# Kernel optimization log

Hardware: AMD Instinct MI355X
Metric: run time of the kernel (lower is better)

The kernel has to match this reference:

```python
import jax, jax.numpy as jnp
import numpy as np

B, N, IN_DIM, H, L = 8, 1024, 3, 256, 3
NUM_STEPS = 200
LN_EPS = 1e-5


def _cdist(a, b):
    # Euclidean pairwise distance, a:[B,n,d], b:[B,m,d] -> [B,n,m]
    d2 = (jnp.sum(a * a, -1)[:, :, None] + jnp.sum(b * b, -1)[:, None, :]
          - 2.0 * jnp.einsum('bik,bjk->bij', a, b))
    d2 = jnp.maximum(d2, 0.0)
    safe = jnp.sqrt(jnp.where(d2 > 0, d2, 1.0))
    return jnp.where(d2 > 0, safe, 0.0)


def _layernorm(x, g, b):
    mu = jnp.mean(x, -1, keepdims=True)
    var = jnp.mean(jnp.square(x - mu), -1, keepdims=True)
    return (x - mu) * jax.lax.rsqrt(var + LN_EPS) * g + b


def setup_inputs() -> dict:
    key = jax.random.key(0)
    ks = jax.random.split(key, 32)
    s = 0.02
    inp = {
        'x': jax.random.normal(ks[0], (B, N, IN_DIM), jnp.float32),
        't': jax.random.randint(ks[1], (B,), 0, NUM_STEPS),
        'mask': jnp.ones((B, N), bool),
        # top-level weights (stored [in,out])
        'w_time': jax.random.normal(ks[2], (1, H)) * s,
        'b_time': jnp.zeros((H,)),
        'w_in': jax.random.normal(ks[3], (IN_DIM + H, H)) * s,
        'b_in': jnp.zeros((H,)),
        'w_out': jax.random.normal(ks[4], (H, IN_DIM)) * s,
        'b_out': jnp.zeros((IN_DIM,)),
        # per-layer stacked params [L, ...]
        'qkv_w': jax.random.normal(ks[5], (L, H, 3 * H)) * s,
        'qkv_b': jnp.zeros((L, 3 * H)),
        'ao_w': jax.random.normal(ks[6], (L, H, H)) * s,
        'ao_b': jnp.zeros((L, H)),
        'fc1_w': jax.random.normal(ks[7], (L, H, 4 * H)) * s,
        'fc1_b': jax.random.normal(ks[8], (L, 4 * H)) * s,
        'fc2_w': jax.random.normal(ks[9], (L, 4 * H, H)) * s,
        'fc2_b': jax.random.normal(ks[10], (L, H)) * s,
        'ln1_g': jnp.ones((L, H)), 'ln1_b': jnp.zeros((L, H)),
        'ln2_g': jnp.ones((L, H)), 'ln2_b': jnp.zeros((L, H)),
    }
    return inp


def reference(x, t, mask, w_time, b_time, w_in, b_in, w_out, b_out,
              qkv_w, qkv_b, ao_w, ao_b, fc1_w, fc1_b, fc2_w, fc2_b,
              ln1_g, ln1_b, ln2_g, ln2_b):
    tf = t.astype(jnp.float32)[:, None] / float(NUM_STEPS)          # [B,1]
    t_embed = jax.nn.relu(tf @ w_time + b_time)                      # [B,H]
    t_embed = jnp.broadcast_to(t_embed[:, None, :], (B, N, H))
    h = jax.nn.relu(jnp.concatenate([x, t_embed], -1) @ w_in + b_in)  # [B,N,H]
    geo = _cdist(h[:, :, :3], h[:, :, :3])                           # [B,N,N]
    mask_f = mask.astype(h.dtype)
    scale = 1.0 / jnp.sqrt(jnp.float32(H))
    for l in range(L):
        qkv = (h @ qkv_w[l] + qkv_b[l]).reshape(B, N, 3, H)
        q, k, v = qkv[:, :, 0], qkv[:, :, 1], qkv[:, :, 2]
        dist = _cdist(geo, geo)                                      # cdist of the distance matrix itself
        scores = jnp.einsum('bik,bjk->bij', q, k) * scale * jnp.exp(-dist)
        scores = jnp.where(mask[:, None, :], scores, -jnp.inf)
        attn = jax.nn.softmax(scores, axis=-1)
        ao = (jnp.einsum('bij,bjk->bik', attn, v) @ ao_w[l] + ao_b[l]) * mask_f[:, :, None]
        xx = _layernorm(h + ao, ln1_g[l], ln1_b[l])
        f1 = jax.nn.relu((xx @ fc1_w[l] + fc1_b[l]) * mask_f[:, :, None])
        ffn = jax.nn.relu((f1 @ fc2_w[l] + fc2_b[l]) * mask_f[:, :, None])
        h = _layernorm(xx + ffn, ln2_g[l], ln2_b[l])
    return (h @ w_out + b_out) * mask_f[:, :, None]
```

## Files before the change

kernel.cpp:

```cpp
#include <hip/hip_runtime.h>
#include <math.h>

#define NB 8
#define NN 1024
#define NH 256
#define NL 3

typedef unsigned short u16;
typedef __bf16 bf16x8 __attribute__((ext_vector_type(8)));
typedef _Float16 f16x8 __attribute__((ext_vector_type(8)));
typedef float f32x4 __attribute__((ext_vector_type(4)));

constexpr int EPI_BIAS_RELU = 2, EPI_BIAS_RELU_RESID = 3, EPI_EDIST = 5, EPI_QKV = 6;

__device__ __forceinline__ unsigned bf16rne(float f) {
    unsigned u = __float_as_uint(f);
    return (u + 0x7fffu + ((u >> 16) & 1u)) >> 16;
}
__device__ __forceinline__ unsigned bfpair(float a, float b) {
    return bf16rne(a) | (bf16rne(b) << 16);
}
__device__ __forceinline__ float bf2f(u16 h) {
    unsigned u = ((unsigned)h) << 16;
    return __uint_as_float(u);
}

__device__ __forceinline__ float blockSum256(float v) {
    __shared__ float sm[4];
    #pragma unroll
    for (int o = 32; o; o >>= 1) v += __shfl_down(v, o, 64);
    int lane = threadIdx.x & 63, wid = threadIdx.x >> 6;
    if (lane == 0) sm[wid] = v;
    __syncthreads();
    if (threadIdx.x == 0) sm[0] = sm[0] + sm[1] + sm[2] + sm[3];
    __syncthreads();
    float r = sm[0];
    __syncthreads();
    return r;
}

template <int EPI, int DT, bool OBF, int SWZ, int MT>
__global__ __launch_bounds__(256) void gemm_mfma(
    const u16* __restrict__ A, int lda, long sA,
    const u16* __restrict__ Bt, int ldb, long sB,
    void* __restrict__ C, int ldc, long sC,
    int K,
    const float* __restrict__ bias, long sBias,
    const float* __restrict__ resid, int ldr,
    u16* __restrict__ vtout)
{
    constexpr int MF = MT / 32;
    constexpr int ASZ = MT * 8;
    __shared__ uint4 sm4[ASZ + 1024];
    const int tid = threadIdx.x;

    int bx = blockIdx.x, by = blockIdx.y, bz = blockIdx.z;
    bool trans = false;
    if (SWZ == 2) {
        int gx = gridDim.x;
        int T = gx * gridDim.y;
        int lid = bx + gx * by;
        int nl = (lid & 7) * (T >> 3) + (lid >> 3);
        bx = nl % gx; by = nl / gx;
    } else if (SWZ == 3) {
        int lid = bx + gridDim.x * bz;
        bz = lid & 7;
        int idx = lid >> 3;
        int j = 0;
        while (idx >= 16 - 2 * j) { idx -= 16 - 2 * j; j++; }
        by = 2 * j + idx;
        bx = j;
        trans = (by >= 2 * bx + 2);
    }
    const int z = bz;
    const int row0 = by * MT, col0 = bx * 128;

    f32x4 acc[MF][4];
    #pragma unroll
    for (int m = 0; m < MF; m++)
        #pragma unroll
        for (int n = 0; n < 4; n++) acc[m][n] = (f32x4){0.f, 0.f, 0.f, 0.f};

    const int l = tid & 63, wid = tid >> 6;
    const int wr = wid >> 1, wc = wid & 1;
    const int lrow = l & 15, lgrp = l >> 4;

    for (int k0 = 0; k0 < K; k0 += 64) {
        if (MT == 128) {
            const int srow = tid >> 1, half = tid & 1, cb = half * 4, swz = srow & 7;
            const u16* Ap = A + (long)z * sA + (long)(row0 + srow) * lda + k0 + half * 32;
            uint4 a0 = *(const uint4*)(Ap + 0),  a1 = *(const uint4*)(Ap + 8);
            uint4 a2 = *(const uint4*)(Ap + 16), a3 = *(const uint4*)(Ap + 24);
            sm4[srow * 8 + ((cb + 0) ^ swz)] = a0;
            sm4[srow * 8 + ((cb + 1) ^ swz)] = a1;
            sm4[srow * 8 + ((cb + 2) ^ swz)] = a2;
            sm4[srow * 8 + ((cb + 3) ^ swz)] = a3;
        } else {
            const int arow = tid >> 2, aq = tid & 3, swz = arow & 7;
            const u16* Ap = A + (long)z * sA + (long)(row0 + arow) * lda + k0 + aq * 16;
            uint4 a0 = *(const uint4*)(Ap + 0), a1 = *(const uint4*)(Ap + 8);
            sm4[arow * 8 + ((aq * 2 + 0) ^ swz)] = a0;
            sm4[arow * 8 + ((aq * 2 + 1) ^ swz)] = a1;
        }
        {
            const int brow = tid >> 1, bq = tid & 1, cb = bq * 4, swz = brow & 7;
            const u16* Bp = Bt + (long)z * sB + (long)(col0 + brow) * ldb + k0 + bq * 32;
            uint4 b0 = *(const uint4*)(Bp + 0),  b1 = *(const uint4*)(Bp + 8);
            uint4 b2 = *(const uint4*)(Bp + 16), b3 = *(const uint4*)(Bp + 24);
            sm4[ASZ + brow * 8 + ((cb + 0) ^ swz)] = b0;
            sm4[ASZ + brow * 8 + ((cb + 1) ^ swz)] = b1;
            sm4[ASZ + brow * 8 + ((cb + 2) ^ swz)] = b2;
            sm4[ASZ + brow * 8 + ((cb + 3) ^ swz)] = b3;
        }
        __syncthreads();

        #pragma unroll
        for (int ks = 0; ks < 2; ks++) {
            int c = ks * 4 + lgrp;
            uint4 a[MF], b[4];
            #pragma unroll
            for (int m = 0; m < MF; m++) {
                int r = wr * (MT / 2) + m * 16 + lrow;
                a[m] = sm4[r * 8 + (c ^ (r & 7))];
            }
            #pragma unroll
            for (int n = 0; n < 4; n++) {
                int r = wc * 64 + n * 16 + lrow;
                b[n] = sm4[ASZ + r * 8 + (c ^ (r & 7))];
            }
            #pragma unroll
            for (int m = 0; m < MF; m++)
                #pragma unroll
                for (int n = 0; n < 4; n++) {
                    if (DT == 0)
                        acc[m][n] = __builtin_amdgcn_mfma_f32_16x16x32_bf16(
                            __builtin_bit_cast(bf16x8, a[m]), __builtin_bit_cast(bf16x8, b[n]), acc[m][n], 0, 0, 0);
                    else
                        acc[m][n] = __builtin_amdgcn_mfma_f32_16x16x32_f16(
                            __builtin_bit_cast(f16x8, a[m]), __builtin_bit_cast(f16x8, b[n]), acc[m][n], 0, 0, 0);
                }
        }
        __syncthreads();
    }

    u16* Ts = (u16*)sm4;
    #pragma unroll
    for (int m = 0; m < MF; m++) {
        #pragma unroll
        for (int n = 0; n < 4; n++) {
            int rbase = row0 + wr * (MT / 2) + m * 16 + lgrp * 4;
            int cc = col0 + wc * 64 + n * 16 + lrow;
            float bv = 0.f;
            if (EPI == EPI_QKV || EPI == EPI_BIAS_RELU || EPI == EPI_BIAS_RELU_RESID)
                bv = bias[cc];
            float vals[4];
            #pragma unroll
            for (int reg = 0; reg < 4; reg++) {
                long r = rbase + reg;
                float v = acc[m][n][reg];
                if (EPI == EPI_QKV) v += bv;
                else if (EPI == EPI_BIAS_RELU) v = fmaxf(v + bv, 0.f);
                else if (EPI == EPI_BIAS_RELU_RESID) v = fmaxf(v + bv, 0.f) + resid[r * ldr + cc];
                else if (EPI == EPI_EDIST) {
                    const float* rnb = bias + (long)z * sBias;
                    float d2 = fmaxf(rnb[r] + rnb[cc] - 2.f * v, 0.f);
                    v = (r == cc) ? 1.f : expf(-sqrtf(d2));
                }
                vals[reg] = v;
                if (OBF) ((u16*)C)[(long)z * sC + r * ldc + cc] = (u16)bf16rne(v);
                else     ((float*)C)[(long)z * sC + r * ldc + cc] = v;
            }
            if (EPI == EPI_EDIST && SWZ == 3 && trans) {
                int cl = cc - col0, rl = rbase - row0;
                uint2 tv;
                tv.x = bfpair(vals[0], vals[1]);
                tv.y = bfpair(vals[2], vals[3]);
                *(uint2*)(Ts + cl * 68 + rl) = tv;
            }
            if (EPI == EPI_QKV && cc >= 512) {
                int b = rbase >> 10;
                uint2 tv;
                tv.x = bfpair(vals[0], vals[1]);
                tv.y = bfpair(vals[2], vals[3]);
                *(uint2*)&vtout[(long)b * NH * NN + (long)(cc - 512) * NN + (rbase & 1023)] = tv;
            }
        }
    }
    if (EPI == EPI_EDIST && SWZ == 3 && trans) {
        __syncthreads();
        int row = tid >> 1, half = tid & 1;
        const u16* src = Ts + row * 68 + half * 32;
        uint2 v0 = *(const uint2*)(src + 0),  v1 = *(const uint2*)(src + 4);
        uint2 v2 = *(const uint2*)(src + 8),  v3 = *(const uint2*)(src + 12);
        uint2 v4 = *(const uint2*)(src + 16), v5 = *(const uint2*)(src + 20);
        uint2 v6 = *(const uint2*)(src + 24), v7 = *(const uint2*)(src + 28);
        uint4* dst = (uint4*)((u16*)C + (long)z * sC + (long)(col0 + row) * ldc + row0 + half * 32);
        uint4 w0 = {v0.x, v0.y, v1.x, v1.y};
        uint4 w1 = {v2.x, v2.y, v3.x, v3.y};
        uint4 w2 = {v4.x, v4.y, v5.x, v5.y};
        uint4 w3 = {v6.x, v6.y, v7.x, v7.y};
        dst[0] = w0; dst[1] = w1; dst[2] = w2; dst[3] = w3;
    }
}

__global__ __launch_bounds__(512) void flash_k(
    const u16* __restrict__ qkv,
    const u16* __restrict__ vt,
    const u16* __restrict__ edist,
    const u16* __restrict__ aow,
    const float* __restrict__ aob,
    const float* __restrict__ hres,
    const float* __restrict__ g1,
    const float* __restrict__ b1,
    float* __restrict__ xb,
    u16* __restrict__ xbbf,
    float scale)
{
    __shared__ uint4 Ks[128][32];
    __shared__ uint4 Vts[256][16];
    __shared__ __align__(16) u16 Es[32][136];
    __shared__ __align__(16) u16 Ps[32][136];
    __shared__ float rs[32][8];
    __shared__ float lnA[32][8];
    __shared__ float lnB[32][8];

    const int tid = threadIdx.x;
    const int l = tid & 63, w = tid >> 6;
    const int g = l >> 4, lr = l & 15;

    int lid = blockIdx.x + gridDim.x * blockIdx.y;
    const int b = lid & 7;
    const int q0 = (lid >> 3) * 32;

    const u16* qkvb = qkv + (long)b * NN * 768;
    const u16* vtb  = vt + (long)b * NH * NN;
    const u16* eb   = edist + (long)b * NN * NN;

    uint4 qf[2][8];
    #pragma unroll
    for (int m = 0; m < 2; m++)
        #pragma unroll
        for (int ks = 0; ks < 8; ks++)
            qf[m][ks] = *(const uint4*)(qkvb + (long)(q0 + 16 * m + lr) * 768 + 32 * ks + 8 * g);

    f32x4 oacc[2][2];
    #pragma unroll
    for (int m = 0; m < 2; m++)
        #pragma unroll
        for (int nf = 0; nf < 2; nf++) oacc[m][nf] = (f32x4){0.f, 0.f, 0.f, 0.f};
    float rsum[2][4] = {{0.f, 0.f, 0.f, 0.f}, {0.f, 0.f, 0.f, 0.f}};

    for (int n0 = 0; n0 < NN; n0 += 128) {
        #pragma unroll
        for (int i = 0; i < 8; i++) {
            int idx = tid + 512 * i;
            int row = idx >> 5, ch = idx & 31;
            Ks[row][ch ^ (row & 7)] = *(const uint4*)(qkvb + (long)(n0 + row) * 768 + 256 + ch * 8);
        }
        #pragma unroll
        for (int i = 0; i < 8; i++) {
            int idx = tid + 512 * i;
            int c = idx >> 4, ch = idx & 15;
            Vts[c][(ch & 8) | ((ch & 7) ^ (c & 7))] = *(const uint4*)(vtb + (long)c * NN + n0 + ch * 8);
        }
        {
            int r = tid >> 4, ch = tid & 15;
            *(uint4*)&Es[r][ch * 8] = *(const uint4*)(eb + (long)(q0 + r) * NN + n0 + ch * 8);
        }
        __syncthreads();

        f32x4 s[2];
        s[0] = (f32x4){0.f, 0.f, 0.f, 0.f};
        s[1] = (f32x4){0.f, 0.f, 0.f, 0.f};
        const int krow = w * 16 + lr;
        #pragma unroll
        for (int ks = 0; ks < 8; ks++) {
            bf16x8 kf = __builtin_bit_cast(bf16x8, Ks[krow][(4 * ks + g) ^ (krow & 7)]);
            s[0] = __builtin_amdgcn_mfma_f32_16x16x32_bf16(__builtin_bit_cast(bf16x8, qf[0][ks]), kf, s[0], 0, 0, 0);
            s[1] = __builtin_amdgcn_mfma_f32_16x16x32_bf16(__builtin_bit_cast(bf16x8, qf[1][ks]), kf, s[1], 0, 0, 0);
        }
        #pragma unroll
        for (int m = 0; m < 2; m++)
            #pragma unroll
            for (int reg = 0; reg < 4; reg++) {
                int q = 16 * m + 4 * g + reg;
                int kc = w * 16 + lr;
                float p = expf(s[m][reg] * scale * bf2f(Es[q][kc]));
                rsum[m][reg] += p;
                Ps[q][kc] = (u16)bf16rne(p);
            }
        __syncthreads();
        #pragma unroll
        for (int ks = 0; ks < 4; ks++) {
            bf16x8 pa[2], vbf[2];
            #pragma unroll
            for (int m = 0; m < 2; m++)
                pa[m] = __builtin_bit_cast(bf16x8, *(const uint4*)&Ps[16 * m + lr][32 * ks + 8 * g]);
            #pragma unroll
            for (int nf = 0; nf < 2; nf++) {
                int c = w * 32 + nf * 16 + lr;
                int ch = 4 * ks + g;
                vbf[nf] = __builtin_bit_cast(bf16x8, Vts[c][(ch & 8) | ((ch & 7) ^ (c & 7))]);
            }
            #pragma unroll
            for (int m = 0; m < 2; m++)
                #pragma unroll
                for (int nf = 0; nf < 2; nf++)
                    oacc[m][nf] = __builtin_amdgcn_mfma_f32_16x16x32_bf16(pa[m], vbf[nf], oacc[m][nf], 0, 0, 0);
        }
        __syncthreads();
    }

    #pragma unroll
    for (int m = 0; m < 2; m++)
        #pragma unroll
        for (int reg = 0; reg < 4; reg++) {
            float v = rsum[m][reg];
            v += __shfl_xor(v, 1); v += __shfl_xor(v, 2);
            v += __shfl_xor(v, 4); v += __shfl_xor(v, 8);
            rsum[m][reg] = v;
        }
    if (lr == 0) {
        #pragma unroll
        for (int m = 0; m < 2; m++)
            #pragma unroll
            for (int reg = 0; reg < 4; reg++)
                rs[16 * m + 4 * g + reg][w] = rsum[m][reg];
    }
    __syncthreads();

    u16* Os = (u16*)Ks;
    #pragma unroll
    for (int m = 0; m < 2; m++)
        #pragma unroll
        for (int reg = 0; reg < 4; reg++) {
            int q = 16 * m + 4 * g + reg;
            float t = 0.f;
            #pragma unroll
            for (int j = 0; j < 8; j++) t += rs[q][j];
            float inv = 1.f / t;
            #pragma unroll
            for (int nf = 0; nf < 2; nf++) {
                int c = w * 32 + nf * 16 + lr;
                Os[q * 264 + c] = (u16)bf16rne(oacc[m][nf][reg] * inv);
            }
        }
    __syncthreads();

    f32x4 aacc[2][2];
    #pragma unroll
    for (int m = 0; m < 2; m++)
        #pragma unroll
        for (int nf = 0; nf < 2; nf++) aacc[m][nf] = (f32x4){0.f, 0.f, 0.f, 0.f};
    #pragma unroll
    for (int kc = 0; kc < 8; kc++) {
        bf16x8 pa[2], wb[2];
        #pragma unroll
        for (int m = 0; m < 2; m++)
            pa[m] = __builtin_bit_cast(bf16x8, *(const uint4*)&Os[(16 * m + lr) * 264 + kc * 32 + 8 * g]);
        #pragma unroll
        for (int nf = 0; nf < 2; nf++)
            wb[nf] = __builtin_bit_cast(bf16x8, *(const uint4*)(aow + (long)(32 * w + 16 * nf + lr) * 256 + kc * 32 + 8 * g));
        #pragma unroll
        for (int m = 0; m < 2; m++)
            #pragma unroll
            for (int nf = 0; nf < 2; nf++)
                aacc[m][nf] = __builtin_amdgcn_mfma_f32_16x16x32_bf16(pa[m], wb[nf], aacc[m][nf], 0, 0, 0);
    }

    int j0 = 32 * w + lr, j1 = 32 * w + 16 + lr;
    float aob0 = aob[j0], aob1 = aob[j1];
    float xv[2][2][4];
    #pragma unroll
    for (int m = 0; m < 2; m++)
        #pragma unroll
        for (int reg = 0; reg < 4; reg++) {
            int q = 16 * m + 4 * g + reg;
            long hr = ((long)b * NN + q0 + q) * NH;
            xv[m][0][reg] = aacc[m][0][reg] + aob0 + hres[hr + j0];
            xv[m][1][reg] = aacc[m][1][reg] + aob1 + hres[hr + j1];
        }

    #pragma unroll
    for (int m = 0; m < 2; m++)
        #pragma unroll
        for (int reg = 0; reg < 4; reg++) {
            float s = xv[m][0][reg] + xv[m][1][reg];
            float s2 = xv[m][0][reg] * xv[m][0][reg] + xv[m][1][reg] * xv[m][1][reg];
            s  += __shfl_xor(s, 1);  s  += __shfl_xor(s, 2);  s  += __shfl_xor(s, 4);  s  += __shfl_xor(s, 8);
            s2 += __shfl_xor(s2, 1); s2 += __shfl_xor(s2, 2); s2 += __shfl_xor(s2, 4); s2 += __shfl_xor(s2, 8);
            if (lr == 0) {
                int q = 16 * m + 4 * g + reg;
                lnA[q][w] = s;
                lnB[q][w] = s2;
            }
        }
    __syncthreads();

    float g1v0 = g1[j0], g1v1 = g1[j1], b1v0 = b1[j0], b1v1 = b1[j1];
    #pragma unroll
    for (int m = 0; m < 2; m++)
        #pragma unroll
        for (int reg = 0; reg < 4; reg++) {
            int q = 16 * m + 4 * g + reg;
            float S = 0.f, S2 = 0.f;
            #pragma unroll
            for (int j = 0; j < 8; j++) { S += lnA[q][j]; S2 += lnB[q][j]; }
            float mu = S * (1.f / NH);
            float var = S2 * (1.f / NH) - mu * mu;
            float rsd = rsqrtf(var + 1e-5f);
            long hr = ((long)b * NN + q0 + q) * NH;
            float o0 = (xv[m][0][reg] - mu) * rsd * g1v0 + b1v0;
            float o1 = (xv[m][1][reg] - mu) * rsd * g1v1 + b1v1;
            xb[hr + j0] = o0;
            xb[hr + j1] = o1;
            xbbf[hr + j0] = (u16)bf16rne(o0);
            xbbf[hr + j1] = (u16)bf16rne(o1);
        }
}

__global__ __launch_bounds__(256) void base_k(const int* __restrict__ t,
                                              const float* __restrict__ w_time,
                                              const float* __restrict__ b_time,
                                              const float* __restrict__ w_in,
                                              const float* __restrict__ b_in,
                                              float* __restrict__ base) {
    int b = blockIdx.x, j = threadIdx.x;
    __shared__ float te[256];
    float tf = (float)t[b] / 200.0f;
    te[j] = fmaxf(tf * w_time[j] + b_time[j], 0.f);
    __syncthreads();
    float acc = b_in[j];
    for (int k = 0; k < 256; k++) acc = fmaf(te[k], w_in[(3 + k) * 256 + j], acc);
    base[b * 256 + j] = acc;
}

__global__ __launch_bounds__(256) void hinit_k(const float* __restrict__ x,
                                               const float* __restrict__ w_in,
                                               const float* __restrict__ base,
                                               float* __restrict__ h,
                                               u16* __restrict__ hbf,
                                               float* __restrict__ h3) {
    long row = blockIdx.x;
    int b = (int)(row >> 10);
    int j = threadIdx.x;
    float x0 = x[row * 3 + 0], x1 = x[row * 3 + 1], x2 = x[row * 3 + 2];
    float v = base[b * 256 + j];
    v = fmaf(x0, w_in[j], v);
    v = fmaf(x1, w_in[256 + j], v);
    v = fmaf(x2, w_in[512 + j], v);
    v = fmaxf(v, 0.f);
    h[row * 256 + j] = v;
    hbf[row * 256 + j] = (u16)bf16rne(v);
    if (j < 3) h3[row * 3 + j] = v;
}

__global__ __launch_bounds__(256) void geo_k(const float* __restrict__ h3,
                                             u16* __restrict__ gf,
                                             float* __restrict__ rn) {
    int bi = blockIdx.x;
    int b = bi >> 10, i = bi & 1023;
    const float* hb = h3 + (long)b * NN * 3;
    float ax = hb[i * 3 + 0], ay = hb[i * 3 + 1], az = hb[i * 3 + 2];
    u16* grow = gf + (long)bi * 1024;
    float accs = 0.f;
    #pragma unroll
    for (int j0 = 0; j0 < NN; j0 += 256) {
        int j = j0 + threadIdx.x;
        float dx = hb[j * 3 + 0] - ax, dy = hb[j * 3 + 1] - ay, dz = hb[j * 3 + 2] - az;
        float d2 = dx * dx + dy * dy + dz * dz;
        float d = (d2 > 0.f) ? sqrtf(d2) : 0.f;
        _Float16 hf = (_Float16)d;
        float rep = (float)hf;
        grow[j] = __builtin_bit_cast(u16, hf);
        accs += rep * rep;
    }
    float tot = blockSum256(accs);
    if (threadIdx.x == 0) rn[bi] = tot;
}

__global__ __launch_bounds__(256) void wtrans_k(const float* __restrict__ qkv_w,
                                                const float* __restrict__ ao_w,
                                                const float* __restrict__ fc1_w,
                                                const float* __restrict__ fc2_w,
                                                u16* __restrict__ qkv_wt,
                                                u16* __restrict__ ao_wt,
                                                u16* __restrict__ fc1_wt,
                                                u16* __restrict__ fc2_wt) {
    int type = blockIdx.z, lyr = blockIdx.y;
    int R, Cc;
    const float* src;
    u16* dst;
    if (type == 0) { R = 256; Cc = 768;  src = qkv_w + (long)lyr * R * Cc; dst = qkv_wt + (long)lyr * R * Cc; }
    else if (type == 1) { R = 256; Cc = 256; src = ao_w + (long)lyr * R * Cc; dst = ao_wt + (long)lyr * R * Cc; }
    else if (type == 2) { R = 256; Cc = 1024; src = fc1_w + (long)lyr * R * Cc; dst = fc1_wt + (long)lyr * R * Cc; }
    else { R = 1024; Cc = 256; src = fc2_w + (long)lyr * R * Cc; dst = fc2_wt + (long)lyr * R * Cc; }
    int tC = Cc >> 5, tR = R >> 5;
    int tile = blockIdx.x;
    if (tile >= tC * tR) return;
    int c0 = (tile % tC) << 5, r0 = (tile / tC) << 5;
    __shared__ float tf[32][33];
    int tx = threadIdx.x & 31, ty = threadIdx.x >> 5;
    #pragma unroll
    for (int i = 0; i < 4; i++) {
        int r = ty + 8 * i;
        tf[r][tx] = src[(long)(r0 + r) * Cc + c0 + tx];
    }
    __syncthreads();
    #pragma unroll
    for (int i = 0; i < 4; i++) {
        int c = ty + 8 * i;
        dst[(long)(c0 + c) * R + r0 + tx] = (u16)bf16rne(tf[tx][c]);
    }
}

__global__ __launch_bounds__(256) void ln_k(float* __restrict__ X,
                                            u16* __restrict__ Xbf,
                                            const float* __restrict__ g,
                                            const float* __restrict__ b) {
    int wid = threadIdx.x >> 6, l = threadIdx.x & 63;
    long row = (long)blockIdx.x * 4 + wid;
    float* p = X + row * NH;
    float4 v = *(float4*)(p + l * 4);
    float s = v.x + v.y + v.z + v.w;
    #pragma unroll
    for (int o = 32; o; o >>= 1) s += __shfl_xor(s, o);
    float mu = s * (1.f / NH);
    float4 d = {v.x - mu, v.y - mu, v.z - mu, v.w - mu};
    float q = d.x * d.x + d.y * d.y + d.z * d.z + d.w * d.w;
    #pragma unroll
    for (int o = 32; o; o >>= 1) q += __shfl_xor(q, o);
    float rsd = rsqrtf(q * (1.f / NH) + 1e-5f);
    float4 g4 = *(const float4*)(g + l * 4);
    float4 b4 = *(const float4*)(b + l * 4);
    float4 o4;
    o4.x = d.x * rsd * g4.x + b4.x;
    o4.y = d.y * rsd * g4.y + b4.y;
    o4.z = d.z * rsd * g4.z + b4.z;
    o4.w = d.w * rsd * g4.w + b4.w;
    *(float4*)(p + l * 4) = o4;
    uint2 pk;
    pk.x = bfpair(o4.x, o4.y);
    pk.y = bfpair(o4.z, o4.w);
    *(uint2*)(Xbf + row * NH + l * 4) = pk;
}

__global__ __launch_bounds__(256) void out_k(const float* __restrict__ h,
                                             const float* __restrict__ w_out,
                                             const float* __restrict__ b_out,
                                             float* __restrict__ out) {
    long row = blockIdx.x;
    int wid = threadIdx.x >> 6, lane = threadIdx.x & 63;
    if (wid < 3) {
        float acc = 0.f;
        for (int k = lane; k < 256; k += 64) acc = fmaf(h[row * 256 + k], w_out[k * 3 + wid], acc);
        #pragma unroll
        for (int o = 32; o; o >>= 1) acc += __shfl_down(acc, o, 64);
        if (lane == 0) out[row * 3 + wid] = acc + b_out[wid];
    }
}

extern "C" void kernel_launch(void* const* d_in, const int* in_sizes, int n_in,
                              void* d_out, int out_size, void* d_ws, size_t ws_size,
                              hipStream_t stream) {
    const float* x      = (const float*)d_in[0];
    const int*   t      = (const int*)  d_in[1];
    const float* w_time = (const float*)d_in[3];
    const float* b_time = (const float*)d_in[4];
    const float* w_in   = (const float*)d_in[5];
    const float* b_in   = (const float*)d_in[6];
    const float* w_out  = (const float*)d_in[7];
    const float* b_out  = (const float*)d_in[8];
    const float* qkv_w  = (const float*)d_in[9];
    const float* qkv_b  = (const float*)d_in[10];
    const float* ao_w   = (const float*)d_in[11];
    const float* ao_b   = (const float*)d_in[12];
    const float* fc1_w  = (const float*)d_in[13];
    const float* fc1_b  = (const float*)d_in[14];
    const float* fc2_w  = (const float*)d_in[15];
    const float* fc2_b  = (const float*)d_in[16];
    const float* ln1_g  = (const float*)d_in[17];
    const float* ln1_b  = (const float*)d_in[18];
    const float* ln2_g  = (const float*)d_in[19];
    const float* ln2_b  = (const float*)d_in[20];
    float* out = (float*)d_out;

    char* W = (char*)d_ws;
    float* h     = (float*)(W);
    float* xb    = (float*)(W + (8ul << 20));
    u16*   hbf   = (u16*)  (W + (16ul << 20));
    u16*   xbbf  = (u16*)  (W + (20ul << 20));
    u16*   vt    = (u16*)  (W + (24ul << 20));
    u16*   f1    = (u16*)  (W + (28ul << 20));
    u16*   qkvb  = (u16*)  (W + (44ul << 20));
    u16*   edist = (u16*)  (W + (56ul << 20));
    u16*   gf    = (u16*)  (W + (72ul << 20));
    u16*   wts   = (u16*)  (W + (88ul << 20));
    u16* qkv_wt = wts;
    u16* ao_wt  = wts + 589824;
    u16* fc1_wt = wts + 786432;
    u16* fc2_wt = wts + 1572864;
    float* base = (float*)(W + (94ul << 20));
    float* rn   = base + 2048;
    float* h3   = rn + 8192;

    const float scale = 1.0f / 16.0f;

    base_k<<<NB, 256, 0, stream>>>(t, w_time, b_time, w_in, b_in, base);
    hinit_k<<<NB * NN, 256, 0, stream>>>(x, w_in, base, h, hbf, h3);
    geo_k<<<NB * NN, 256, 0, stream>>>(h3, gf, rn);
    wtrans_k<<<dim3(256, NL, 4), 256, 0, stream>>>(qkv_w, ao_w, fc1_w, fc2_w,
                                                   qkv_wt, ao_wt, fc1_wt, fc2_wt);
    gemm_mfma<EPI_EDIST, 1, true, 3, 64><<<dim3(72, 1, 8), 256, 0, stream>>>(
        gf, 1024, (long)NN * 1024, gf, 1024, (long)NN * 1024,
        edist, NN, (long)NN * NN, 1024, rn, NN, nullptr, 0, nullptr);

    for (int l = 0; l < NL; ++l) {
        gemm_mfma<EPI_QKV, 0, true, 2, 128><<<dim3(6, 64, 1), 256, 0, stream>>>(
            hbf, NH, 0, qkv_wt + (long)l * 196608, NH, 0, qkvb, 768, 0,
            NH, qkv_b + l * 768, 0, nullptr, 0, vt);
        flash_k<<<dim3(32, 8), 512, 0, stream>>>(
            qkvb, vt, edist, ao_wt + (long)l * 65536, ao_b + l * NH,
            h, ln1_g + l * NH, ln1_b + l * NH, xb, xbbf, scale);
        gemm_mfma<EPI_BIAS_RELU, 0, true, 2, 128><<<dim3(8, 64, 1), 256, 0, stream>>>(
            xbbf, NH, 0, fc1_wt + (long)l * 262144, NH, 0, f1, 1024, 0,
            NH, fc1_b + l * 1024, 0, nullptr, 0, nullptr);
        gemm_mfma<EPI_BIAS_RELU_RESID, 0, false, 2, 64><<<dim3(2, 128, 1), 256, 0, stream>>>(
            f1, 1024, 0, fc2_wt + (long)l * 262144, 1024, 0, h, NH, 0,
            1024, fc2_b + l * NH, 0, xb, NH, nullptr);
        ln_k<<<2048, 256, 0, stream>>>(h, hbf, ln2_g + l * NH, ln2_b + l * NH);
    }
    out_k<<<NB * NN, 256, 0, stream>>>(h, w_out, b_out, out);
}
```

Measured before the change: 331.9 us.

## Fuse FC2 GEMM with LayerNorm and read K/V directly from global in attention

Replaces the FC2 GEMM plus separate LayerNorm kernel with a single fc2ln_k kernel. Each 32-row block computes the full 256-wide output, adds bias, ReLU and residual, then applies LayerNorm in registers, which removes the fp32 round trip through h and one launch per layer. The flash attention kernel drops the shared-memory staging of K and V^T and loads MFMA fragments straight from global/L2, which also removes one barrier per tile. The QKV GEMM tile shrinks from 128 to 64 rows. The risks are uncoalesced, redundant global reads of K/V across waves, only 256 blocks for FC2, and a one-pass variance that is slightly less numerically robust.

```diff
diff --git a/kernel.cpp b/kernel.cpp
--- a/kernel.cpp
+++ b/kernel.cpp
@@ -11,7 +11,7 @@
 typedef _Float16 f16x8 __attribute__((ext_vector_type(8)));
 typedef float f32x4 __attribute__((ext_vector_type(4)));
 
-constexpr int EPI_BIAS_RELU = 2, EPI_BIAS_RELU_RESID = 3, EPI_EDIST = 5, EPI_QKV = 6;
+constexpr int EPI_BIAS_RELU = 2, EPI_EDIST = 5, EPI_QKV = 6;
 
 __device__ __forceinline__ unsigned bf16rne(float f) {
     unsigned u = __float_as_uint(f);
@@ -46,7 +46,6 @@
     void* __restrict__ C, int ldc, long sC,
     int K,
     const float* __restrict__ bias, long sBias,
-    const float* __restrict__ resid, int ldr,
     u16* __restrict__ vtout)
 {
     constexpr int MF = MT / 32;
@@ -151,7 +150,7 @@
             int rbase = row0 + wr * (MT / 2) + m * 16 + lgrp * 4;
             int cc = col0 + wc * 64 + n * 16 + lrow;
             float bv = 0.f;
-            if (EPI == EPI_QKV || EPI == EPI_BIAS_RELU || EPI == EPI_BIAS_RELU_RESID)
+            if (EPI == EPI_QKV || EPI == EPI_BIAS_RELU)
                 bv = bias[cc];
             float vals[4];
             #pragma unroll
@@ -160,7 +159,6 @@
                 float v = acc[m][n][reg];
                 if (EPI == EPI_QKV) v += bv;
                 else if (EPI == EPI_BIAS_RELU) v = fmaxf(v + bv, 0.f);
-                else if (EPI == EPI_BIAS_RELU_RESID) v = fmaxf(v + bv, 0.f) + resid[r * ldr + cc];
                 else if (EPI == EPI_EDIST) {
                     const float* rnb = bias + (long)z * sBias;
                     float d2 = fmaxf(rnb[r] + rnb[cc] - 2.f * v, 0.f);
@@ -216,10 +214,9 @@
     u16* __restrict__ xbbf,
     float scale)
 {
-    __shared__ uint4 Ks[128][32];
-    __shared__ uint4 Vts[256][16];
     __shared__ __align__(16) u16 Es[32][136];
     __shared__ __align__(16) u16 Ps[32][136];
+    __shared__ __align__(16) u16 Os[32 * 264];
     __shared__ float rs[32][8];
     __shared__ float lnA[32][8];
     __shared__ float lnB[32][8];
@@ -251,18 +248,6 @@
     float rsum[2][4] = {{0.f, 0.f, 0.f, 0.f}, {0.f, 0.f, 0.f, 0.f}};
 
     for (int n0 = 0; n0 < NN; n0 += 128) {
-        #pragma unroll
-        for (int i = 0; i < 8; i++) {
-            int idx = tid + 512 * i;
-            int row = idx >> 5, ch = idx & 31;
-            Ks[row][ch ^ (row & 7)] = *(const uint4*)(qkvb + (long)(n0 + row) * 768 + 256 + ch * 8);
-        }
-        #pragma unroll
-        for (int i = 0; i < 8; i++) {
-            int idx = tid + 512 * i;
-            int c = idx >> 4, ch = idx & 15;
-            Vts[c][(ch & 8) | ((ch & 7) ^ (c & 7))] = *(const uint4*)(vtb + (long)c * NN + n0 + ch * 8);
-        }
         {
             int r = tid >> 4, ch = tid & 15;
             *(uint4*)&Es[r][ch * 8] = *(const uint4*)(eb + (long)(q0 + r) * NN + n0 + ch * 8);
@@ -272,10 +257,10 @@
         f32x4 s[2];
         s[0] = (f32x4){0.f, 0.f, 0.f, 0.f};
         s[1] = (f32x4){0.f, 0.f, 0.f, 0.f};
-        const int krow = w * 16 + lr;
+        const u16* kbase = qkvb + (long)(n0 + w * 16 + lr) * 768 + 256;
         #pragma unroll
         for (int ks = 0; ks < 8; ks++) {
-            bf16x8 kf = __builtin_bit_cast(bf16x8, Ks[krow][(4 * ks + g) ^ (krow & 7)]);
+            bf16x8 kf = __builtin_bit_cast(bf16x8, *(const uint4*)(kbase + 32 * ks + 8 * g));
             s[0] = __builtin_amdgcn_mfma_f32_16x16x32_bf16(__builtin_bit_cast(bf16x8, qf[0][ks]), kf, s[0], 0, 0, 0);
             s[1] = __builtin_amdgcn_mfma_f32_16x16x32_bf16(__builtin_bit_cast(bf16x8, qf[1][ks]), kf, s[1], 0, 0, 0);
         }
@@ -290,6 +275,7 @@
                 Ps[q][kc] = (u16)bf16rne(p);
             }
         __syncthreads();
+
         #pragma unroll
         for (int ks = 0; ks < 4; ks++) {
             bf16x8 pa[2], vbf[2];
@@ -299,8 +285,7 @@
             #pragma unroll
             for (int nf = 0; nf < 2; nf++) {
                 int c = w * 32 + nf * 16 + lr;
-                int ch = 4 * ks + g;
-                vbf[nf] = __builtin_bit_cast(bf16x8, Vts[c][(ch & 8) | ((ch & 7) ^ (c & 7))]);
+                vbf[nf] = __builtin_bit_cast(bf16x8, *(const uint4*)(vtb + (long)c * NN + n0 + 32 * ks + 8 * g));
             }
             #pragma unroll
             for (int m = 0; m < 2; m++)
@@ -308,7 +293,6 @@
                 for (int nf = 0; nf < 2; nf++)
                     oacc[m][nf] = __builtin_amdgcn_mfma_f32_16x16x32_bf16(pa[m], vbf[nf], oacc[m][nf], 0, 0, 0);
         }
-        __syncthreads();
     }
 
     #pragma unroll
@@ -329,7 +313,6 @@
     }
     __syncthreads();
 
-    u16* Os = (u16*)Ks;
     #pragma unroll
     for (int m = 0; m < 2; m++)
         #pragma unroll
@@ -416,6 +399,121 @@
             xb[hr + j1] = o1;
             xbbf[hr + j0] = (u16)bf16rne(o0);
             xbbf[hr + j1] = (u16)bf16rne(o1);
+        }
+}
+
+__global__ __launch_bounds__(256) void fc2ln_k(
+    const u16* __restrict__ f1,
+    const float* __restrict__ resid,
+    const u16* __restrict__ w2,
+    const float* __restrict__ b2,
+    const float* __restrict__ g2,
+    const float* __restrict__ bb2,
+    float* __restrict__ hout,
+    u16* __restrict__ hbf)
+{
+    __shared__ uint4 As[256];
+    __shared__ uint4 Bs[2048];
+    __shared__ float lnA[32][4], lnB[32][4];
+
+    const int tid = threadIdx.x;
+    const int l = tid & 63, w = tid >> 6;
+    const int lrow = l & 15, lgrp = l >> 4;
+    const long r0 = (long)blockIdx.x * 32;
+
+    f32x4 acc[2][4];
+    #pragma unroll
+    for (int m = 0; m < 2; m++)
+        #pragma unroll
+        for (int n = 0; n < 4; n++) acc[m][n] = (f32x4){0.f, 0.f, 0.f, 0.f};
+
+    for (int k0 = 0; k0 < 1024; k0 += 64) {
+        {
+            int row = tid >> 3, ch = tid & 7;
+            As[row * 8 + (ch ^ (row & 7))] = *(const uint4*)(f1 + (r0 + row) * 1024 + k0 + ch * 8);
+        }
+        #pragma unroll
+        for (int i = 0; i < 8; i++) {
+            int idx = tid + 256 * i;
+            int row = idx >> 3, ch = idx & 7;
+            Bs[row * 8 + (ch ^ (row & 7))] = *(const uint4*)(w2 + (long)row * 1024 + k0 + ch * 8);
+        }
+        __syncthreads();
+        #pragma unroll
+        for (int ks = 0; ks < 2; ks++) {
+            int c = ks * 4 + lgrp;
+            uint4 a[2], b[4];
+            #pragma unroll
+            for (int m = 0; m < 2; m++) {
+                int r = m * 16 + lrow;
+                a[m] = As[r * 8 + (c ^ (r & 7))];
+            }
+            #pragma unroll
+            for (int n = 0; n < 4; n++) {
+                int r = 64 * w + n * 16 + lrow;
+                b[n] = Bs[r * 8 + (c ^ (r & 7))];
+            }
+            #pragma unroll
+            for (int m = 0; m < 2; m++)
+                #pragma unroll
+                for (int n = 0; n < 4; n++)
+                    acc[m][n] = __builtin_amdgcn_mfma_f32_16x16x32_bf16(
+                        __builtin_bit_cast(bf16x8, a[m]), __builtin_bit_cast(bf16x8, b[n]), acc[m][n], 0, 0, 0);
+        }
+        __syncthreads();
+    }
+
+    float xv[2][4][4];
+    #pragma unroll
+    for (int m = 0; m < 2; m++)
+        #pragma unroll
+        for (int n = 0; n < 4; n++) {
+            int cc = 64 * w + 16 * n + lrow;
+            float bv = b2[cc];
+            #pragma unroll
+            for (int reg = 0; reg < 4; reg++) {
+                int rr = 16 * m + 4 * lgrp + reg;
+                xv[m][n][reg] = fmaxf(acc[m][n][reg] + bv, 0.f) + resid[(r0 + rr) * 256 + cc];
+            }
+        }
+
+    #pragma unroll
+    for (int m = 0; m < 2; m++)
+        #pragma unroll
+        for (int reg = 0; reg < 4; reg++) {
+            float s = 0.f, s2 = 0.f;
+            #pragma unroll
+            for (int n = 0; n < 4; n++) {
+                s += xv[m][n][reg];
+                s2 += xv[m][n][reg] * xv[m][n][reg];
+            }
+            s  += __shfl_xor(s, 1);  s  += __shfl_xor(s, 2);  s  += __shfl_xor(s, 4);  s  += __shfl_xor(s, 8);
+            s2 += __shfl_xor(s2, 1); s2 += __shfl_xor(s2, 2); s2 += __shfl_xor(s2, 4); s2 += __shfl_xor(s2, 8);
+            if (lrow == 0) {
+                int rr = 16 * m + 4 * lgrp + reg;
+                lnA[rr][w] = s;
+                lnB[rr][w] = s2;
+            }
+        }
+    __syncthreads();
+
+    #pragma unroll
+    for (int m = 0; m < 2; m++)
+        #pragma unroll
+        for (int reg = 0; reg < 4; reg++) {
+            int rr = 16 * m + 4 * lgrp + reg;
+            float S = lnA[rr][0] + lnA[rr][1] + lnA[rr][2] + lnA[rr][3];
+            float S2 = lnB[rr][0] + lnB[rr][1] + lnB[rr][2] + lnB[rr][3];
+            float mu = S * (1.f / NH);
+            float var = S2 * (1.f / NH) - mu * mu;
+            float rsd = rsqrtf(var + 1e-5f);
+            #pragma unroll
+            for (int n = 0; n < 4; n++) {
+                int cc = 64 * w + 16 * n + lrow;
+                float o = (xv[m][n][reg] - mu) * rsd * g2[cc] + bb2[cc];
+                hout[(r0 + rr) * 256 + cc] = o;
+                hbf[(r0 + rr) * 256 + cc] = (u16)bf16rne(o);
+            }
         }
 }
 
@@ -512,37 +610,6 @@
         int c = ty + 8 * i;
         dst[(long)(c0 + c) * R + r0 + tx] = (u16)bf16rne(tf[tx][c]);
     }
-}
-
-__global__ __launch_bounds__(256) void ln_k(float* __restrict__ X,
-                                            u16* __restrict__ Xbf,
-                                            const float* __restrict__ g,
-                                            const float* __restrict__ b) {
-    int wid = threadIdx.x >> 6, l = threadIdx.x & 63;
-    long row = (long)blockIdx.x * 4 + wid;
-    float* p = X + row * NH;
-    float4 v = *(float4*)(p + l * 4);
-    float s = v.x + v.y + v.z + v.w;
-    #pragma unroll
-    for (int o = 32; o; o >>= 1) s += __shfl_xor(s, o);
-    float mu = s * (1.f / NH);
-    float4 d = {v.x - mu, v.y - mu, v.z - mu, v.w - mu};
-    float q = d.x * d.x + d.y * d.y + d.z * d.z + d.w * d.w;
-    #pragma unroll
-    for (int o = 32; o; o >>= 1) q += __shfl_xor(q, o);
-    float rsd = rsqrtf(q * (1.f / NH) + 1e-5f);
-    float4 g4 = *(const float4*)(g + l * 4);
-    float4 b4 = *(const float4*)(b + l * 4);
-    float4 o4;
-    o4.x = d.x * rsd * g4.x + b4.x;
-    o4.y = d.y * rsd * g4.y + b4.y;
-    o4.z = d.z * rsd * g4.z + b4.z;
-    o4.w = d.w * rsd * g4.w + b4.w;
-    *(float4*)(p + l * 4) = o4;
-    uint2 pk;
-    pk.x = bfpair(o4.x, o4.y);
-    pk.y = bfpair(o4.z, o4.w);
-    *(uint2*)(Xbf + row * NH + l * 4) = pk;
 }
 
 __global__ __launch_bounds__(256) void out_k(const float* __restrict__ h,
@@ -613,22 +680,21 @@
                                                    qkv_wt, ao_wt, fc1_wt, fc2_wt);
     gemm_mfma<EPI_EDIST, 1, true, 3, 64><<<dim3(72, 1, 8), 256, 0, stream>>>(
         gf, 1024, (long)NN * 1024, gf, 1024, (long)NN * 1024,
-        edist, NN, (long)NN * NN, 1024, rn, NN, nullptr, 0, nullptr);
+        edist, NN, (long)NN * NN, 1024, rn, NN, nullptr);
 
     for (int l = 0; l < NL; ++l) {
-        gemm_mfma<EPI_QKV, 0, true, 2, 128><<<dim3(6, 64, 1), 256, 0, stream>>>(
+        gemm_mfma<EPI_QKV, 0, true, 2, 64><<<dim3(6, 128, 1), 256, 0, stream>>>(
             hbf, NH, 0, qkv_wt + (long)l * 196608, NH, 0, qkvb, 768, 0,
-            NH, qkv_b + l * 768, 0, nullptr, 0, vt);
+            NH, qkv_b + l * 768, 0, vt);
         flash_k<<<dim3(32, 8), 512, 0, stream>>>(
             qkvb, vt, edist, ao_wt + (long)l * 65536, ao_b + l * NH,
             h, ln1_g + l * NH, ln1_b + l * NH, xb, xbbf, scale);
         gemm_mfma<EPI_BIAS_RELU, 0, true, 2, 128><<<dim3(8, 64, 1), 256, 0, stream>>>(
             xbbf, NH, 0, fc1_wt + (long)l * 262144, NH, 0, f1, 1024, 0,
-            NH, fc1_b + l * 1024, 0, nullptr, 0, nullptr);
-        gemm_mfma<EPI_BIAS_RELU_RESID, 0, false, 2, 64><<<dim3(2, 128, 1), 256, 0, stream>>>(
-            f1, 1024, 0, fc2_wt + (long)l * 262144, 1024, 0, h, NH, 0,
-            1024, fc2_b + l * NH, 0, xb, NH, nullptr);
-        ln_k<<<2048, 256, 0, stream>>>(h, hbf, ln2_g + l * NH, ln2_b + l * NH);
+            NH, fc1_b + l * 1024, 0, nullptr);
+        fc2ln_k<<<256, 256, 0, stream>>>(
+            f1, xb, fc2_wt + (long)l * 262144, fc2_b + l * NH,
+            ln2_g + l * NH, ln2_b + l * NH, h, hbf);
     }
     out_k<<<NB * NN, 256, 0, stream>>>(h, w_out, b_out, out);
 }
```

After: 360.3 us. 1.09x slower.
